# Optimization experiments

Hardware: AMD Instinct MI355X
Metric: run time of the kernel (lower is better)

Reference implementation:

```python
import jax, jax.numpy as jnp
import numpy as np

N_ATOMS = 8192
N_FINGERPRINT = 10000
DIM = 64
N_LAYERS = 3
N_MOL = 256


def setup_inputs() -> dict:
    key = jax.random.key(0)
    k1, k2, k3, k4, k5 = jax.random.split(key, 5)
    fingerprints = jax.random.randint(k1, (N_ATOMS,), 0, N_FINGERPRINT)
    adjacencies = jax.random.uniform(k2, (N_ATOMS, N_ATOMS), dtype=jnp.float32)
    segment_ids = jnp.sort(jax.random.randint(k3, (N_ATOMS,), 0, N_MOL))
    embed_table = jax.random.normal(k4, (N_FINGERPRINT, DIM), dtype=jnp.float32) * 0.1
    W = jax.random.normal(k5, (N_LAYERS, DIM, DIM), dtype=jnp.float32) * (1.0 / np.sqrt(DIM))
    b = jnp.zeros((N_LAYERS, DIM), dtype=jnp.float32)
    return {"fingerprints": fingerprints, "adjacencies": adjacencies,
            "segment_ids": segment_ids, "embed_table": embed_table, "W": W, "b": b}


def reference(fingerprints, adjacencies, segment_ids, embed_table, W, b):
    # Embed fingerprint indices -> [N_atoms, dim]
    vectors = embed_table[fingerprints]
    # MPNN layers: h = relu(Linear(v)); v = h + A @ h  (residual message passing)
    for layer in range(N_LAYERS):
        h = jax.nn.relu(jnp.einsum('nd,ed->ne', vectors, W[layer]) + b[layer])
        vectors = h + adjacencies @ h
    # Sum pooling per molecule (torch.split + sum == segment_sum over sorted ids)
    molecular_vectors = jax.ops.segment_sum(vectors, segment_ids, num_segments=N_MOL)
    return molecular_vectors
```

## Files before the change

kernel.cpp:

```cpp
#include <hip/hip_runtime.h>

#define N_ATOMS 8192
#define DIM 64
#define N_MOL 256
#define N_LAYERS 3
#define KS 16
#define KCH (N_ATOMS / KS)
#define BM 128
#define BN 64
#define BK 64
#define NSTEP (KCH / BK)

typedef __attribute__((ext_vector_type(8))) short short8v;
typedef __attribute__((ext_vector_type(4))) float f32x4;
typedef unsigned short ushort_t;

__device__ __forceinline__ ushort_t f2bf(float x) {
    unsigned u = __float_as_uint(x);
    u += 0x7fffu + ((u >> 16) & 1u);
    return (ushort_t)(u >> 16);
}

__device__ __forceinline__ void gload16(const void* gsrc, void* ldst) {
    __builtin_amdgcn_global_load_lds(
        (const __attribute__((address_space(1))) void*)gsrc,
        (__attribute__((address_space(3))) void*)ldst, 16, 0, 0);
}

__global__ void embed_kernel(const int* __restrict__ fp,
                             const float* __restrict__ table,
                             float* __restrict__ v) {
    int n = blockIdx.x;
    int d = threadIdx.x;
    v[n * DIM + d] = table[fp[n] * DIM + d];
}

__global__ __launch_bounds__(256) void linear_relu_T_kernel(
        const float* __restrict__ v, const float* __restrict__ W,
        const float* __restrict__ b, float* __restrict__ vnext,
        ushort_t* __restrict__ hT) {
    __shared__ float Ws[DIM][DIM + 1];
    __shared__ float vsT[DIM][68];

    const int t = threadIdx.x;
    const int n0 = blockIdx.x * 64;
    for (int i = t; i < DIM * DIM; i += 256) {
        Ws[i >> 6][i & 63] = W[i];
        float val = v[n0 * DIM + i];
        vsT[i & 63][i >> 6] = val;
    }
    __syncthreads();

    const int e = t & 63;
    const int g = t >> 6;
    float acc[16];
    const float be = b[e];
#pragma unroll
    for (int i = 0; i < 16; ++i) acc[i] = be;

    for (int d = 0; d < DIM; ++d) {
        const float w = Ws[e][d];
        const float4* vp = (const float4*)&vsT[d][g * 16];
        float4 x0 = vp[0], x1 = vp[1], x2 = vp[2], x3 = vp[3];
        acc[0]  += w * x0.x; acc[1]  += w * x0.y; acc[2]  += w * x0.z; acc[3]  += w * x0.w;
        acc[4]  += w * x1.x; acc[5]  += w * x1.y; acc[6]  += w * x1.z; acc[7]  += w * x1.w;
        acc[8]  += w * x2.x; acc[9]  += w * x2.y; acc[10] += w * x2.z; acc[11] += w * x2.w;
        acc[12] += w * x3.x; acc[13] += w * x3.y; acc[14] += w * x3.z; acc[15] += w * x3.w;
    }

    ushort_t hb[16];
#pragma unroll
    for (int i = 0; i < 16; ++i) {
        float hv = acc[i] > 0.f ? acc[i] : 0.f;
        const int n = n0 + g * 16 + i;
        vnext[(size_t)n * DIM + e] = hv;
        hb[i] = f2bf(hv);
    }
    ushort_t* hp = hT + (size_t)e * N_ATOMS + n0 + g * 16;
    *(short8v*)(hp)     = *(short8v*)&hb[0];
    *(short8v*)(hp + 8) = *(short8v*)&hb[8];
}

template <int CVT>
__global__ __launch_bounds__(256) void matmul_mfma_kernel(
        const float* __restrict__ A, const ushort_t* __restrict__ Abf_in,
        ushort_t* __restrict__ Abf_out, const ushort_t* __restrict__ hT,
        float* __restrict__ pbuf) {
    __shared__ ushort_t Asw[2][BM * BK];
    __shared__ ushort_t Bsw[2][BN * BK];

    const int t  = threadIdx.x;
    const int w  = t >> 6;
    const int l  = t & 63;
    const int lm = l & 15;
    const int lq = l >> 4;
    const int r0 = blockIdx.x * BM;
    const size_t kc0 = (size_t)blockIdx.y * KCH;

    auto stage = [&](int bi, size_t kb) {
        if (CVT) {
#pragma unroll
            for (int q = 0; q < 4; ++q) {
                const int i = q * 256 + t;
                const int r = i >> 3, s = i & 7;
                const size_t goff = (size_t)(r0 + r) * N_ATOMS + kb + s * 8;
                const float4* g = (const float4*)(A + goff);
                float4 a0 = g[0], a1 = g[1];
                short8v vv;
                vv[0] = (short)f2bf(a0.x); vv[1] = (short)f2bf(a0.y);
                vv[2] = (short)f2bf(a0.z); vv[3] = (short)f2bf(a0.w);
                vv[4] = (short)f2bf(a1.x); vv[5] = (short)f2bf(a1.y);
                vv[6] = (short)f2bf(a1.z); vv[7] = (short)f2bf(a1.w);
                *(short8v*)&Asw[bi][r * BK + ((s ^ (r & 7)) << 3)] = vv;
                *(short8v*)(Abf_out + goff) = vv;
            }
        } else {
#pragma unroll
            for (int q = 0; q < 4; ++q) {
                const int i = q * 256 + t;
                const int r = i >> 3, s = i & 7;
                gload16(Abf_in + (size_t)(r0 + r) * N_ATOMS + kb + ((s ^ (r & 7)) << 3),
                        &Asw[bi][(q * 256 + w * 64) * 8]);
            }
        }
#pragma unroll
        for (int q = 0; q < 2; ++q) {
            const int i = q * 256 + t;
            const int r = i >> 3, s = i & 7;
            gload16(hT + (size_t)r * N_ATOMS + kb + ((s ^ (r & 7)) << 3),
                    &Bsw[bi][(q * 256 + w * 64) * 8]);
        }
    };

    f32x4 acc[2][4];
#pragma unroll
    for (int m = 0; m < 2; ++m)
#pragma unroll
        for (int n = 0; n < 4; ++n) acc[m][n] = (f32x4){0.f, 0.f, 0.f, 0.f};

    stage(0, kc0);
    __syncthreads();

    for (int ks = 0; ks < NSTEP; ++ks) {
        const int bi = ks & 1;
        if (ks + 1 < NSTEP) stage(bi ^ 1, kc0 + (size_t)(ks + 1) * BK);
#pragma unroll
        for (int kki = 0; kki < 2; ++kki) {
            const int sx = ((lq + kki * 4) ^ (lm & 7)) << 3;
            const int ra = w * 32 + lm;
            short8v a0 = *(const short8v*)&Asw[bi][ra * BK + sx];
            short8v a1 = *(const short8v*)&Asw[bi][(ra + 16) * BK + sx];
            short8v b0 = *(const short8v*)&Bsw[bi][(lm)      * BK + sx];
            short8v b1 = *(const short8v*)&Bsw[bi][(lm + 16) * BK + sx];
            short8v b2 = *(const short8v*)&Bsw[bi][(lm + 32) * BK + sx];
            short8v b3 = *(const short8v*)&Bsw[bi][(lm + 48) * BK + sx];
            acc[0][0] = __builtin_amdgcn_mfma_f32_16x16x32_bf16(a0, b0, acc[0][0], 0, 0, 0);
            acc[0][1] = __builtin_amdgcn_mfma_f32_16x16x32_bf16(a0, b1, acc[0][1], 0, 0, 0);
            acc[0][2] = __builtin_amdgcn_mfma_f32_16x16x32_bf16(a0, b2, acc[0][2], 0, 0, 0);
            acc[0][3] = __builtin_amdgcn_mfma_f32_16x16x32_bf16(a0, b3, acc[0][3], 0, 0, 0);
            acc[1][0] = __builtin_amdgcn_mfma_f32_16x16x32_bf16(a1, b0, acc[1][0], 0, 0, 0);
            acc[1][1] = __builtin_amdgcn_mfma_f32_16x16x32_bf16(a1, b1, acc[1][1], 0, 0, 0);
            acc[1][2] = __builtin_amdgcn_mfma_f32_16x16x32_bf16(a1, b2, acc[1][2], 0, 0, 0);
            acc[1][3] = __builtin_amdgcn_mfma_f32_16x16x32_bf16(a1, b3, acc[1][3], 0, 0, 0);
        }
        __syncthreads();
    }

    float* pb = pbuf + (size_t)blockIdx.y * ((size_t)N_ATOMS * DIM);
    const int rb = r0 + w * 32 + lq * 4;
#pragma unroll
    for (int m = 0; m < 2; ++m)
#pragma unroll
        for (int j = 0; j < 4; ++j) {
            float* vp = pb + (size_t)(rb + m * 16 + j) * DIM + lm;
#pragma unroll
            for (int n = 0; n < 4; ++n) vp[n * 16] = acc[m][n][j];
        }
}

__global__ __launch_bounds__(256) void reduce_kernel(
        const float* __restrict__ pbuf, float* __restrict__ vnext) {
    const size_t i = ((size_t)blockIdx.x * 256 + threadIdx.x) * 4;
    f32x4 s = *(const f32x4*)(vnext + i);
#pragma unroll
    for (int sp = 0; sp < KS; ++sp)
        s += *(const f32x4*)(pbuf + (size_t)sp * (N_ATOMS * DIM) + i);
    *(f32x4*)(vnext + i) = s;
}

__device__ __forceinline__ int lower_bound_dev(const int* __restrict__ seg, int val) {
    int lo = 0, hi = N_ATOMS;
    while (lo < hi) {
        int mid = (lo + hi) >> 1;
        if (seg[mid] < val) lo = mid + 1; else hi = mid;
    }
    return lo;
}

__global__ void segsum_kernel(const float* __restrict__ v,
                              const int* __restrict__ seg,
                              float* __restrict__ out) {
    int m = blockIdx.x;
    int d = threadIdx.x;
    int lo = lower_bound_dev(seg, m);
    int hi = lower_bound_dev(seg, m + 1);
    float acc = 0.f;
    for (int n = lo; n < hi; ++n) acc += v[n * DIM + d];
    out[m * DIM + d] = acc;
}

extern "C" void kernel_launch(void* const* d_in, const int* in_sizes, int n_in,
                              void* d_out, int out_size, void* d_ws, size_t ws_size,
                              hipStream_t stream) {
    const int*   fp    = (const int*)d_in[0];
    const float* A     = (const float*)d_in[1];
    const int*   seg   = (const int*)d_in[2];
    const float* table = (const float*)d_in[3];
    const float* W     = (const float*)d_in[4];
    const float* b     = (const float*)d_in[5];
    float* out = (float*)d_out;

    float*    v0   = (float*)d_ws;
    float*    v1   = v0 + (size_t)N_ATOMS * DIM;
    float*    pbuf = v1 + (size_t)N_ATOMS * DIM;
    ushort_t* hT   = (ushort_t*)(pbuf + (size_t)KS * N_ATOMS * DIM);
    ushort_t* Abf  = hT + (size_t)DIM * N_ATOMS;

    embed_kernel<<<N_ATOMS, DIM, 0, stream>>>(fp, table, v0);

    float* vcur = v0;
    float* vnext = v1;
    for (int l = 0; l < N_LAYERS; ++l) {
        linear_relu_T_kernel<<<N_ATOMS / 64, 256, 0, stream>>>(
            vcur, W + l * DIM * DIM, b + l * DIM, vnext, hT);
        dim3 grid(N_ATOMS / BM, KS);
        if (l == 0)
            matmul_mfma_kernel<1><<<grid, 256, 0, stream>>>(A, Abf, Abf, hT, pbuf);
        else
            matmul_mfma_kernel<0><<<grid, 256, 0, stream>>>(A, Abf, Abf, hT, pbuf);
        reduce_kernel<<<(N_ATOMS * DIM) / (256 * 4), 256, 0, stream>>>(pbuf, vnext);
        float* tmp = vcur; vcur = vnext; vnext = tmp;
    }

    segsum_kernel<<<N_MOL, DIM, 0, stream>>>(vcur, seg, out);
}
```

Baseline: 229.1 us.

## Fuse split-K reduction and embedding into linear and segment-sum kernels

Removes the separate embed and split-K reduce kernels. The embedding gather now happens inside the first linear kernel, and the partial-sum reduction over the split-K buffers happens when the next linear layer or the final segment sum loads its input. This saves several launches and one full write and read of the activation array per layer. The linear kernel now handles 32 rows per block instead of 64, giving more blocks. The segment sum uses 4 row groups per block, and each thread now reads 16 partial buffers inline, which may raise load latency in those kernels.

```diff
diff --git a/kernel.cpp b/kernel.cpp
--- a/kernel.cpp
+++ b/kernel.cpp
@@ -27,58 +27,57 @@
         (__attribute__((address_space(3))) void*)ldst, 16, 0, 0);
 }
 
-__global__ void embed_kernel(const int* __restrict__ fp,
-                             const float* __restrict__ table,
-                             float* __restrict__ v) {
-    int n = blockIdx.x;
-    int d = threadIdx.x;
-    v[n * DIM + d] = table[fp[n] * DIM + d];
-}
-
-__global__ __launch_bounds__(256) void linear_relu_T_kernel(
-        const float* __restrict__ v, const float* __restrict__ W,
-        const float* __restrict__ b, float* __restrict__ vnext,
-        ushort_t* __restrict__ hT) {
+template <int FIRST>
+__global__ __launch_bounds__(256) void fused_linear_kernel(
+        const int* __restrict__ fp, const float* __restrict__ table,
+        const float* __restrict__ hprev, const float* __restrict__ pbuf,
+        const float* __restrict__ W, const float* __restrict__ b,
+        float* __restrict__ hout, ushort_t* __restrict__ hT) {
     __shared__ float Ws[DIM][DIM + 1];
-    __shared__ float vsT[DIM][68];
+    __shared__ float vsT[DIM][36];
 
     const int t = threadIdx.x;
-    const int n0 = blockIdx.x * 64;
-    for (int i = t; i < DIM * DIM; i += 256) {
-        Ws[i >> 6][i & 63] = W[i];
-        float val = v[n0 * DIM + i];
-        vsT[i & 63][i >> 6] = val;
+    const int n0 = blockIdx.x * 32;
+    for (int i = t; i < DIM * DIM; i += 256) Ws[i >> 6][i & 63] = W[i];
+    for (int i = t; i < 32 * DIM; i += 256) {
+        const int nl = i >> 6, d = i & 63;
+        const size_t n = n0 + nl;
+        float val;
+        if (FIRST) {
+            val = table[(size_t)fp[n] * DIM + d];
+        } else {
+            val = hprev[n * DIM + d];
+#pragma unroll
+            for (int sp = 0; sp < KS; ++sp)
+                val += pbuf[(size_t)sp * (N_ATOMS * DIM) + n * DIM + d];
+        }
+        vsT[d][nl] = val;
     }
     __syncthreads();
 
     const int e = t & 63;
     const int g = t >> 6;
-    float acc[16];
+    float acc[8];
     const float be = b[e];
 #pragma unroll
-    for (int i = 0; i < 16; ++i) acc[i] = be;
+    for (int i = 0; i < 8; ++i) acc[i] = be;
 
     for (int d = 0; d < DIM; ++d) {
         const float w = Ws[e][d];
-        const float4* vp = (const float4*)&vsT[d][g * 16];
-        float4 x0 = vp[0], x1 = vp[1], x2 = vp[2], x3 = vp[3];
-        acc[0]  += w * x0.x; acc[1]  += w * x0.y; acc[2]  += w * x0.z; acc[3]  += w * x0.w;
-        acc[4]  += w * x1.x; acc[5]  += w * x1.y; acc[6]  += w * x1.z; acc[7]  += w * x1.w;
-        acc[8]  += w * x2.x; acc[9]  += w * x2.y; acc[10] += w * x2.z; acc[11] += w * x2.w;
-        acc[12] += w * x3.x; acc[13] += w * x3.y; acc[14] += w * x3.z; acc[15] += w * x3.w;
-    }
-
-    ushort_t hb[16];
-#pragma unroll
-    for (int i = 0; i < 16; ++i) {
+        const float4* vp = (const float4*)&vsT[d][g * 8];
+        float4 x0 = vp[0], x1 = vp[1];
+        acc[0] += w * x0.x; acc[1] += w * x0.y; acc[2] += w * x0.z; acc[3] += w * x0.w;
+        acc[4] += w * x1.x; acc[5] += w * x1.y; acc[6] += w * x1.z; acc[7] += w * x1.w;
+    }
+
+    ushort_t hb[8];
+#pragma unroll
+    for (int i = 0; i < 8; ++i) {
         float hv = acc[i] > 0.f ? acc[i] : 0.f;
-        const int n = n0 + g * 16 + i;
-        vnext[(size_t)n * DIM + e] = hv;
+        hout[(size_t)(n0 + g * 8 + i) * DIM + e] = hv;
         hb[i] = f2bf(hv);
     }
-    ushort_t* hp = hT + (size_t)e * N_ATOMS + n0 + g * 16;
-    *(short8v*)(hp)     = *(short8v*)&hb[0];
-    *(short8v*)(hp + 8) = *(short8v*)&hb[8];
+    *(short8v*)(hT + (size_t)e * N_ATOMS + n0 + g * 8) = *(short8v*)&hb[0];
 }
 
 template <int CVT>
@@ -178,16 +177,6 @@
         }
 }
 
-__global__ __launch_bounds__(256) void reduce_kernel(
-        const float* __restrict__ pbuf, float* __restrict__ vnext) {
-    const size_t i = ((size_t)blockIdx.x * 256 + threadIdx.x) * 4;
-    f32x4 s = *(const f32x4*)(vnext + i);
-#pragma unroll
-    for (int sp = 0; sp < KS; ++sp)
-        s += *(const f32x4*)(pbuf + (size_t)sp * (N_ATOMS * DIM) + i);
-    *(f32x4*)(vnext + i) = s;
-}
-
 __device__ __forceinline__ int lower_bound_dev(const int* __restrict__ seg, int val) {
     int lo = 0, hi = N_ATOMS;
     while (lo < hi) {
@@ -197,16 +186,26 @@
     return lo;
 }
 
-__global__ void segsum_kernel(const float* __restrict__ v,
-                              const int* __restrict__ seg,
-                              float* __restrict__ out) {
-    int m = blockIdx.x;
-    int d = threadIdx.x;
-    int lo = lower_bound_dev(seg, m);
-    int hi = lower_bound_dev(seg, m + 1);
+__global__ __launch_bounds__(256) void fused_segsum_kernel(
+        const float* __restrict__ h, const float* __restrict__ pbuf,
+        const int* __restrict__ seg, float* __restrict__ out) {
+    __shared__ float sm[4][DIM];
+    const int m = blockIdx.x;
+    const int d = threadIdx.x & 63;
+    const int g = threadIdx.x >> 6;
+    const int lo = lower_bound_dev(seg, m);
+    const int hi = lower_bound_dev(seg, m + 1);
     float acc = 0.f;
-    for (int n = lo; n < hi; ++n) acc += v[n * DIM + d];
-    out[m * DIM + d] = acc;
+    for (int n = lo + g; n < hi; n += 4) {
+        float v = h[(size_t)n * DIM + d];
+#pragma unroll
+        for (int sp = 0; sp < KS; ++sp)
+            v += pbuf[(size_t)sp * (N_ATOMS * DIM) + (size_t)n * DIM + d];
+        acc += v;
+    }
+    sm[g][d] = acc;
+    __syncthreads();
+    if (g == 0) out[(size_t)m * DIM + d] = sm[0][d] + sm[1][d] + sm[2][d] + sm[3][d];
 }
 
 extern "C" void kernel_launch(void* const* d_in, const int* in_sizes, int n_in,
@@ -220,27 +219,22 @@
     const float* b     = (const float*)d_in[5];
     float* out = (float*)d_out;
 
-    float*    v0   = (float*)d_ws;
-    float*    v1   = v0 + (size_t)N_ATOMS * DIM;
-    float*    pbuf = v1 + (size_t)N_ATOMS * DIM;
+    float*    h0   = (float*)d_ws;
+    float*    h1   = h0 + (size_t)N_ATOMS * DIM;
+    float*    pbuf = h1 + (size_t)N_ATOMS * DIM;
     ushort_t* hT   = (ushort_t*)(pbuf + (size_t)KS * N_ATOMS * DIM);
     ushort_t* Abf  = hT + (size_t)DIM * N_ATOMS;
 
-    embed_kernel<<<N_ATOMS, DIM, 0, stream>>>(fp, table, v0);
-
-    float* vcur = v0;
-    float* vnext = v1;
-    for (int l = 0; l < N_LAYERS; ++l) {
-        linear_relu_T_kernel<<<N_ATOMS / 64, 256, 0, stream>>>(
-            vcur, W + l * DIM * DIM, b + l * DIM, vnext, hT);
-        dim3 grid(N_ATOMS / BM, KS);
-        if (l == 0)
-            matmul_mfma_kernel<1><<<grid, 256, 0, stream>>>(A, Abf, Abf, hT, pbuf);
-        else
-            matmul_mfma_kernel<0><<<grid, 256, 0, stream>>>(A, Abf, Abf, hT, pbuf);
-        reduce_kernel<<<(N_ATOMS * DIM) / (256 * 4), 256, 0, stream>>>(pbuf, vnext);
-        float* tmp = vcur; vcur = vnext; vnext = tmp;
-    }
-
-    segsum_kernel<<<N_MOL, DIM, 0, stream>>>(vcur, seg, out);
-}
+    dim3 mmgrid(N_ATOMS / BM, KS);
+
+    fused_linear_kernel<1><<<N_ATOMS / 32, 256, 0, stream>>>(
+        fp, table, nullptr, pbuf, W, b, h0, hT);
+    matmul_mfma_kernel<1><<<mmgrid, 256, 0, stream>>>(A, Abf, Abf, hT, pbuf);
+    fused_linear_kernel<0><<<N_ATOMS / 32, 256, 0, stream>>>(
+        fp, table, h0, pbuf, W + DIM * DIM, b + DIM, h1, hT);
+    matmul_mfma_kernel<0><<<mmgrid, 256, 0, stream>>>(A, Abf, Abf, hT, pbuf);
+    fused_linear_kernel<0><<<N_ATOMS / 32, 256, 0, stream>>>(
+        fp, table, h1, pbuf, W + 2 * DIM * DIM, b + 2 * DIM, h0, hT);
+    matmul_mfma_kernel<0><<<mmgrid, 256, 0, stream>>>(A, Abf, Abf, hT, pbuf);
+    fused_segsum_kernel<<<N_MOL, 256, 0, stream>>>(h0, pbuf, seg, out);
+}
```

Measured after the change: 221.9 us. 3.1% less time.
